# Kernel tuning notes

Hardware: AMD Instinct MI355X
Metric: run time of the kernel (lower is better)

## Reference

```python
import jax, jax.numpy as jnp
import numpy as np

B, S, H, V = 4, 2048, 768, 32000
HID = 100          # self.hidden_size
N_LABELS = 3
LN2 = 0.6931471805599453


def setup_inputs() -> dict:
    key = jax.random.key(0)
    ks = jax.random.split(key, 10)
    return {
        "input_ids": jax.random.randint(ks[0], (B, S), 0, V),
        "attention_mask": jnp.ones((B, S), jnp.float32),
        "sentiment": jax.random.normal(ks[1], (B, 3), jnp.float32),
        "hidden_states": jax.random.normal(ks[2], (B, S, H), jnp.float32),
        "lm_logits": jax.random.normal(ks[3], (B, S, V), jnp.float32),
        "W_ih": jax.random.normal(ks[4], (4 * HID, H + 1), jnp.float32) * 0.05,
        "W_hh": jax.random.normal(ks[5], (4 * HID, HID), jnp.float32) * 0.05,
        "b_ih": jax.random.normal(ks[6], (4 * HID,), jnp.float32) * 0.05,
        "b_hh": jax.random.normal(ks[7], (4 * HID,), jnp.float32) * 0.05,
        "cls_W": jax.random.normal(ks[8], (N_LABELS, HID + 3), jnp.float32) * 0.05,
        "cls_b": jax.random.normal(ks[9], (N_LABELS,), jnp.float32) * 0.05,
    }


def _lstm_last(x, W_ih, W_hh, b_ih, b_hh):
    # x: [B,S,D] -> last hidden state [B,HID]; PyTorch gate order i,f,g,o
    b, hid = x.shape[0], W_hh.shape[1]
    x_proj = jnp.einsum('bsd,gd->bsg', x, W_ih) + b_ih + b_hh  # [B,S,4H]

    def step(carry, xt):
        h, c = carry
        gates = xt + h @ W_hh.T
        i, f, g, o = jnp.split(gates, 4, axis=-1)
        c = jax.nn.sigmoid(f) * c + jax.nn.sigmoid(i) * jnp.tanh(g)
        h = jax.nn.sigmoid(o) * jnp.tanh(c)
        return (h, c), None

    h0 = jnp.zeros((b, hid), x.dtype)
    (hT, _), _ = jax.lax.scan(step, (h0, h0), jnp.swapaxes(x_proj, 0, 1))
    return hT


def reference(input_ids, attention_mask, sentiment, hidden_states, lm_logits,
              W_ih, W_hh, b_ih, b_hh, cls_W, cls_b):
    # surprisal: -log2(softmax(logits)[input_ids]) * mask, detached
    log_p = jax.nn.log_softmax(lm_logits, axis=-1)                       # [B,S,V]
    lp = jnp.take_along_axis(log_p, input_ids[..., None], axis=2)[..., 0]  # [B,S]
    surp = jax.lax.stop_gradient((-lp / LN2) * attention_mask)

    x = jnp.concatenate([hidden_states, surp[..., None]], axis=-1)  # [B,S,H+1]
    hT = _lstm_last(x, W_ih, W_hh, b_ih, b_hh)                      # [B,HID]
    # dropout is identity at inference
    feat = jnp.concatenate([hT, sentiment], axis=1)                 # [B,HID+3]
    return feat @ cls_W.T + cls_b                                   # [B,N_LABELS]
```

## Files before the change

### kernel.cpp

```cpp
#include <hip/hip_runtime.h>
#include <hip/hip_bf16.h>
#include <math.h>

#define B 4
#define S 2048
#define H 768
#define V 32000
#define HID 100
#define G4 400
#define M_TOT (B*S)
#define PD 2

typedef _Float16 half2_t __attribute__((ext_vector_type(2)));
typedef _Float16 half8_t __attribute__((ext_vector_type(8)));

__device__ __forceinline__ float fdot2_(half2_t a, half2_t b, float c) {
#if __has_builtin(__builtin_amdgcn_fdot2)
  return __builtin_amdgcn_fdot2(a, b, c, false);
#else
  return c + (float)a[0] * (float)b[0] + (float)a[1] * (float)b[1];
#endif
}

__device__ __forceinline__ float sigmoidf_(float x) {
  return 1.0f / (1.0f + __expf(-x));
}

__device__ __forceinline__ void lds_barrier_() {
  asm volatile("s_waitcnt lgkmcnt(0)" ::: "memory");
  __builtin_amdgcn_s_barrier();
  asm volatile("" ::: "memory");
}

__global__ __launch_bounds__(256) void surprisal_kernel(
    const float* __restrict__ logits, const int* __restrict__ ids,
    const float* __restrict__ mask, float* __restrict__ surp) {
  int row = blockIdx.x;
  const float* x = logits + (size_t)row * V;
  int tid = threadIdx.x;
  float m = -INFINITY, s = 0.0f;
  const float4* x4 = (const float4*)x;
  for (int i = tid; i < V / 4; i += 256) {
    float4 v = x4[i];
    float mv = fmaxf(fmaxf(v.x, v.y), fmaxf(v.z, v.w));
    if (mv > m) { s *= __expf(m - mv); m = mv; }
    s += __expf(v.x - m) + __expf(v.y - m) + __expf(v.z - m) + __expf(v.w - m);
  }
  #pragma unroll
  for (int off = 32; off > 0; off >>= 1) {
    float mo = __shfl_xor(m, off);
    float so = __shfl_xor(s, off);
    float mn = fmaxf(m, mo);
    s = s * __expf(m - mn) + so * __expf(mo - mn);
    m = mn;
  }
  __shared__ float sm[4], ss[4];
  int wid = tid >> 6, lane = tid & 63;
  if (lane == 0) { sm[wid] = m; ss[wid] = s; }
  __syncthreads();
  if (tid == 0) {
    float M = sm[0], Ssum = ss[0];
    #pragma unroll
    for (int w = 1; w < 4; ++w) {
      float mo = sm[w], so = ss[w];
      float mn = fmaxf(M, mo);
      Ssum = Ssum * __expf(M - mn) + so * __expf(mo - mn);
      M = mn;
    }
    float xid = x[ids[row]];
    surp[row] = (M + __logf(Ssum) - xid) * 1.4426950408889634f * mask[row];
  }
}

#define BM 64
#define BN 64
#define BK 32

__global__ __launch_bounds__(256) void xproj_kernel(
    const float* __restrict__ A,
    const float* __restrict__ surp,
    const float* __restrict__ W,
    const float* __restrict__ b_ih, const float* __restrict__ b_hh,
    float* __restrict__ xproj) {
  __shared__ float As[BK][BM];
  __shared__ float Bs[BK][BN];
  int tid = threadIdx.x;
  int m0 = blockIdx.x * BM;
  int n0 = blockIdx.y * BN;
  int tx = tid & 15, ty = tid >> 4;
  float acc[4][4] = {};
  for (int k0 = 0; k0 < H; k0 += BK) {
    #pragma unroll
    for (int l = 0; l < 2; ++l) {
      int idx = tid + l * 256;
      int row = idx >> 3;
      int kq = idx & 7;
      float4 v = *(const float4*)&A[(size_t)(m0 + row) * H + k0 + kq * 4];
      As[kq * 4 + 0][row] = v.x;
      As[kq * 4 + 1][row] = v.y;
      As[kq * 4 + 2][row] = v.z;
      As[kq * 4 + 3][row] = v.w;
    }
    #pragma unroll
    for (int l = 0; l < 8; ++l) {
      int idx = tid + l * 256;
      int n = idx >> 5;
      int kk = idx & 31;
      int gn = n0 + n;
      Bs[kk][n] = (gn < G4) ? W[(size_t)gn * (H + 1) + k0 + kk] : 0.0f;
    }
    __syncthreads();
    #pragma unroll
    for (int k = 0; k < BK; ++k) {
      float4 a = *(const float4*)&As[k][ty * 4];
      float4 bq = *(const float4*)&Bs[k][tx * 4];
      float av[4] = {a.x, a.y, a.z, a.w};
      float bv[4] = {bq.x, bq.y, bq.z, bq.w};
      #pragma unroll
      for (int i = 0; i < 4; ++i)
        #pragma unroll
        for (int j = 0; j < 4; ++j)
          acc[i][j] += av[i] * bv[j];
    }
    __syncthreads();
  }
  #pragma unroll
  for (int i = 0; i < 4; ++i) {
    int gm = m0 + ty * 4 + i;
    float sv = surp[gm];
    #pragma unroll
    for (int j = 0; j < 4; ++j) {
      int gn = n0 + tx * 4 + j;
      if (gn < G4) {
        float val = acc[i][j] + sv * W[(size_t)gn * (H + 1) + H] + b_ih[gn] + b_hh[gn];
        int pn = 4 * (gn % HID) + gn / HID;
        xproj[(size_t)gm * G4 + pn] = val;
      }
    }
  }
}

#define NH2 52
__global__ __launch_bounds__(448, 1) void lstm_kernel(
    const float* __restrict__ xproj,
    const float* __restrict__ W_hh,
    const float* __restrict__ sent,
    const float* __restrict__ cls_W,
    const float* __restrict__ cls_b,
    float* __restrict__ out) {
  int b = blockIdx.x;
  int tid = threadIdx.x;
  __shared__ __align__(16) _Float16 hb0[2 * NH2];
  __shared__ __align__(16) _Float16 hb1[2 * NH2];

  bool active = tid < G4;
  int p = active ? tid : (G4 - 1);
  int k = p >> 2, g = p & 3;
  int r = g * HID + k;
  bool is_g = (g == 2);

  half2_t w[NH2];
  {
    const float* wr = W_hh + (size_t)r * HID;
    #pragma unroll
    for (int j = 0; j < 50; ++j)
      w[j] = half2_t{(_Float16)wr[2 * j], (_Float16)wr[2 * j + 1]};
    #pragma unroll
    for (int j = 50; j < NH2; ++j) w[j] = half2_t{0, 0};
  }

  float c_reg = 0.0f;
  if (tid < 2 * NH2) { hb0[tid] = (_Float16)0; hb1[tid] = (_Float16)0; }
  __syncthreads();

  const float* xp = xproj + (size_t)b * S * G4;
  float xr[PD];
  #pragma unroll
  for (int d = 0; d < PD; ++d) xr[d] = xp[(size_t)d * G4 + p];

  #pragma unroll 2
  for (int t = 0; t < S; ++t) {
    int slot = t & (PD - 1);
    const half8_t* hr = (t & 1) ? (const half8_t*)hb0 : (const half8_t*)hb1;
    _Float16* hw = (t & 1) ? hb1 : hb0;

    float a0 = 0.f, a1 = 0.f;
    #pragma unroll
    for (int j = 0; j < 13; ++j) {
      half8_t hv = hr[j];
      half2_t h0 = {hv[0], hv[1]}, h1 = {hv[2], hv[3]};
      half2_t h2 = {hv[4], hv[5]}, h3 = {hv[6], hv[7]};
      a0 = fdot2_(w[4 * j + 0], h0, a0);
      a1 = fdot2_(w[4 * j + 1], h1, a1);
      a0 = fdot2_(w[4 * j + 2], h2, a0);
      a1 = fdot2_(w[4 * j + 3], h3, a1);
    }
    float a = a0 + a1 + xr[slot];

    {
      int tp = (t + PD < S) ? (t + PD) : (S - 1);
      xr[slot] = xp[(size_t)tp * G4 + p];
    }

    float xa = is_g ? 2.0f * a : a;
    float sg = sigmoidf_(xa);
    float val = is_g ? (2.0f * sg - 1.0f) : sg;

    float vf = __shfl_xor(val, 1);
    float vg = __shfl_xor(val, 2);
    float vo = __shfl_xor(vf, 2);

    c_reg = vf * c_reg + val * vg;
    float tc = 2.0f * sigmoidf_(2.0f * c_reg) - 1.0f;
    float h = vo * tc;
    if (active && g == 0) hw[k] = (_Float16)h;

    lds_barrier_();
  }

  if (tid < 3) {
    float acc = cls_b[tid];
    const float* cw = cls_W + tid * (HID + 3);
    #pragma unroll
    for (int j = 0; j < HID; ++j) acc += cw[j] * (float)hb1[j];
    #pragma unroll
    for (int k2 = 0; k2 < 3; ++k2) acc += cw[HID + k2] * sent[b * 3 + k2];
    out[b * 3 + tid] = acc;
  }
}

extern "C" void kernel_launch(void* const* d_in, const int* in_sizes, int n_in,
                              void* d_out, int out_size, void* d_ws, size_t ws_size,
                              hipStream_t stream) {
  const int*   input_ids = (const int*)d_in[0];
  const float* mask      = (const float*)d_in[1];
  const float* sent      = (const float*)d_in[2];
  const float* hs        = (const float*)d_in[3];
  const float* logits    = (const float*)d_in[4];
  const float* W_ih      = (const float*)d_in[5];
  const float* W_hh      = (const float*)d_in[6];
  const float* b_ih      = (const float*)d_in[7];
  const float* b_hh      = (const float*)d_in[8];
  const float* cls_W     = (const float*)d_in[9];
  const float* cls_b     = (const float*)d_in[10];
  float* out = (float*)d_out;

  float* surp  = (float*)d_ws;
  float* xproj = surp + M_TOT;

  surprisal_kernel<<<M_TOT, 256, 0, stream>>>(logits, input_ids, mask, surp);
  xproj_kernel<<<dim3(M_TOT / BM, (G4 + BN - 1) / BN), 256, 0, stream>>>(
      hs, surp, W_ih, b_ih, b_hh, xproj);
  lstm_kernel<<<B, 448, 0, stream>>>(xproj, W_hh, sent, cls_W, cls_b, out);
}
```

Baseline: 1.515 ms.

## Assign two LSTM gates per thread to shrink recurrent block to four waves

```diff
diff --git a/kernel.cpp b/kernel.cpp
--- a/kernel.cpp
+++ b/kernel.cpp
@@ -133,7 +133,8 @@
       int gn = n0 + tx * 4 + j;
       if (gn < G4) {
         float val = acc[i][j] + sv * W[(size_t)gn * (H + 1) + H] + b_ih[gn] + b_hh[gn];
-        int pn = 4 * (gn % HID) + gn / HID;
+        int g = gn / HID, k = gn % HID;
+        int pn = 4 * k + (((g & 1) << 1) | (g >> 1));
         xproj[(size_t)gm * G4 + pn] = val;
       }
     }
@@ -141,7 +142,7 @@
 }
 
 #define NH2 52
-__global__ __launch_bounds__(448, 1) void lstm_kernel(
+__global__ __launch_bounds__(256, 1) void lstm_kernel(
     const float* __restrict__ xproj,
     const float* __restrict__ W_hh,
     const float* __restrict__ sent,
@@ -153,20 +154,24 @@
   __shared__ __align__(16) _Float16 hb0[2 * NH2];
   __shared__ __align__(16) _Float16 hb1[2 * NH2];
 
-  bool active = tid < G4;
-  int p = active ? tid : (G4 - 1);
-  int k = p >> 2, g = p & 3;
-  int r = g * HID + k;
-  bool is_g = (g == 2);
-
-  half2_t w[NH2];
+  bool active = tid < 200;
+  int q = active ? tid : 199;
+  int k = q >> 1;
+  bool odd = (q & 1) != 0;
+  int rA = odd ? (HID + k) : k;
+  int rB = odd ? (3 * HID + k) : (2 * HID + k);
+
+  half2_t wA[NH2], wB[NH2];
   {
-    const float* wr = W_hh + (size_t)r * HID;
-    #pragma unroll
-    for (int j = 0; j < 50; ++j)
-      w[j] = half2_t{(_Float16)wr[2 * j], (_Float16)wr[2 * j + 1]};
-    #pragma unroll
-    for (int j = 50; j < NH2; ++j) w[j] = half2_t{0, 0};
+    const float* pA = W_hh + (size_t)rA * HID;
+    const float* pB = W_hh + (size_t)rB * HID;
+    #pragma unroll
+    for (int j = 0; j < 50; ++j) {
+      wA[j] = half2_t{(_Float16)pA[2 * j], (_Float16)pA[2 * j + 1]};
+      wB[j] = half2_t{(_Float16)pB[2 * j], (_Float16)pB[2 * j + 1]};
+    }
+    #pragma unroll
+    for (int j = 50; j < NH2; ++j) { wA[j] = half2_t{0, 0}; wB[j] = half2_t{0, 0}; }
   }
 
   float c_reg = 0.0f;
@@ -174,9 +179,10 @@
   __syncthreads();
 
   const float* xp = xproj + (size_t)b * S * G4;
-  float xr[PD];
+  float2 xr[PD];
   #pragma unroll
-  for (int d = 0; d < PD; ++d) xr[d] = xp[(size_t)d * G4 + p];
+  for (int d = 0; d < PD; ++d)
+    xr[d] = ((const float2*)(xp + (size_t)d * G4))[q];
 
   #pragma unroll 2
   for (int t = 0; t < S; ++t) {
@@ -184,36 +190,41 @@
     const half8_t* hr = (t & 1) ? (const half8_t*)hb0 : (const half8_t*)hb1;
     _Float16* hw = (t & 1) ? hb1 : hb0;
 
-    float a0 = 0.f, a1 = 0.f;
+    float2 xv = xr[slot];
+    {
+      int tp = (t + PD < S) ? (t + PD) : (S - 1);
+      xr[slot] = ((const float2*)(xp + (size_t)tp * G4))[q];
+    }
+
+    float a0 = 0.f, a1 = 0.f, b0 = 0.f, b1 = 0.f;
     #pragma unroll
     for (int j = 0; j < 13; ++j) {
       half8_t hv = hr[j];
       half2_t h0 = {hv[0], hv[1]}, h1 = {hv[2], hv[3]};
       half2_t h2 = {hv[4], hv[5]}, h3 = {hv[6], hv[7]};
-      a0 = fdot2_(w[4 * j + 0], h0, a0);
-      a1 = fdot2_(w[4 * j + 1], h1, a1);
-      a0 = fdot2_(w[4 * j + 2], h2, a0);
-      a1 = fdot2_(w[4 * j + 3], h3, a1);
-    }
-    float a = a0 + a1 + xr[slot];
-
-    {
-      int tp = (t + PD < S) ? (t + PD) : (S - 1);
-      xr[slot] = xp[(size_t)tp * G4 + p];
-    }
-
-    float xa = is_g ? 2.0f * a : a;
-    float sg = sigmoidf_(xa);
-    float val = is_g ? (2.0f * sg - 1.0f) : sg;
-
-    float vf = __shfl_xor(val, 1);
-    float vg = __shfl_xor(val, 2);
-    float vo = __shfl_xor(vf, 2);
-
-    c_reg = vf * c_reg + val * vg;
+      a0 = fdot2_(wA[4 * j + 0], h0, a0);
+      b0 = fdot2_(wB[4 * j + 0], h0, b0);
+      a1 = fdot2_(wA[4 * j + 1], h1, a1);
+      b1 = fdot2_(wB[4 * j + 1], h1, b1);
+      a0 = fdot2_(wA[4 * j + 2], h2, a0);
+      b0 = fdot2_(wB[4 * j + 2], h2, b0);
+      a1 = fdot2_(wA[4 * j + 3], h3, a1);
+      b1 = fdot2_(wB[4 * j + 3], h3, b1);
+    }
+    float aA = a0 + a1 + xv.x;
+    float aB = b0 + b1 + xv.y;
+
+    float vA = sigmoidf_(aA);
+    float sB = sigmoidf_(odd ? aB : 2.0f * aB);
+    float vB = odd ? sB : (2.0f * sB - 1.0f);
+
+    float f_n = __shfl_xor(vA, 1);
+    float o_n = __shfl_xor(vB, 1);
+
+    c_reg = f_n * c_reg + vA * vB;
     float tc = 2.0f * sigmoidf_(2.0f * c_reg) - 1.0f;
-    float h = vo * tc;
-    if (active && g == 0) hw[k] = (_Float16)h;
+    float h = o_n * tc;
+    if (active && !odd) hw[k] = (_Float16)h;
 
     lds_barrier_();
   }
@@ -251,5 +262,5 @@
   surprisal_kernel<<<M_TOT, 256, 0, stream>>>(logits, input_ids, mask, surp);
   xproj_kernel<<<dim3(M_TOT / BM, (G4 + BN - 1) / BN), 256, 0, stream>>>(
       hs, surp, W_ih, b_ih, b_hh, xproj);
-  lstm_kernel<<<B, 448, 0, stream>>>(xproj, W_hh, sent, cls_W, cls_b, out);
-}
+  lstm_kernel<<<B, 256, 0, stream>>>(xproj, W_hh, sent, cls_W, cls_b, out);
+}
```

After: 1.403 ms. 7.4% less time.
